# Kernel optimization log

Measured on AMD Instinct MI355X. Metric: run time of the kernel, lower is better.

## Reference

```python
import jax, jax.numpy as jnp
import numpy as np
from jax import lax

B, C, H, W = 4, 256, 64, 64
C8 = C // 8  # 32


def setup_inputs() -> dict:
    key = jax.random.key(0)
    ks = jax.random.split(key, 8)
    x = jax.random.normal(ks[0], (B, C, H, W), jnp.float32)
    # 1x1 conv weights stored as [out_ch, in_ch]
    wb = jax.random.normal(ks[1], (C8, 2 * C), jnp.float32) * 0.02
    bb = jax.random.normal(ks[2], (C8,), jnp.float32) * 0.02
    wc = jax.random.normal(ks[3], (C8, 2 * C), jnp.float32) * 0.02
    bc = jax.random.normal(ks[4], (C8,), jnp.float32) * 0.02
    wd = jax.random.normal(ks[5], (C, 2 * C), jnp.float32) * 0.02
    bd = jax.random.normal(ks[6], (C,), jnp.float32) * 0.02
    alpha = jnp.float32(0.5)  # nn.Parameter(zeros(1)) at init; nonzero for a meaningful test
    return {"x": x, "wb": wb, "bb": bb, "wc": wc, "bc": bc, "wd": wd, "bd": bd, "alpha": alpha}


def reference(x, wb, bb, wc, bc, wd, bd, alpha):
    b, c, h, w = x.shape
    n = h * w
    pad = [(0, 0), (0, 0), (1, 1), (1, 1)]
    # F.avg_pool2d(k=3, s=1, p=1) with count_include_pad=True -> window-sum / 9
    x_avg = lax.reduce_window(x, 0.0, lax.add, (1, 1, 3, 3), (1, 1, 1, 1), pad) / 9.0
    x_max = lax.reduce_window(x, -jnp.inf, lax.max, (1, 1, 3, 3), (1, 1, 1, 1), pad)
    cat = jnp.concatenate([x_avg, x_max], axis=1)  # [B, 2C, H, W]
    catf = cat.reshape(b, 2 * c, n)                # [B, 2C, N]
    # 1x1 convs == per-pixel linear projections
    feat_b = jnp.einsum('oc,bcn->bon', wb, catf) + bb[None, :, None]  # [B, C8, N]
    feat_c = jnp.einsum('oc,bcn->bon', wc, catf) + bc[None, :, None]  # [B, C8, N]
    feat_d = jnp.einsum('oc,bcn->bon', wd, catf) + bd[None, :, None]  # [B, C,  N]
    # attention_s = softmax(feat_b^T @ feat_c) over last dim -> [B, N, N]
    attn = jax.nn.softmax(jnp.einsum('bon,bom->bnm', feat_b, feat_c), axis=-1)
    # feat_e = feat_d @ attn^T -> [B, C, N]
    feat_e = jnp.einsum('bcn,bmn->bcm', feat_d, attn).reshape(b, c, h, w)
    return alpha * feat_e + (1.0 - alpha) * x
```

## Files before the change

kernel.cpp:

```cpp
#include <hip/hip_runtime.h>
#include <hip/hip_bf16.h>

typedef __hip_bfloat16 bf16;
typedef __attribute__((ext_vector_type(8))) short s8v;
typedef __attribute__((ext_vector_type(4))) float f4v;

__device__ __forceinline__ ushort f2u(float f) {
    bf16 h = __float2bfloat16(f);
    return *(ushort*)&h;
}


__global__ __launch_bounds__(256) void pool_kernel(const float* __restrict__ x,
                                                   ushort* __restrict__ cat) {
    __shared__ float Xs[3][64][66];
    int tid = threadIdx.x;
    int bid = blockIdx.x;
    int b = bid >> 8, h = (bid >> 2) & 63, cg = bid & 3;
    bool hasU = (h > 0), hasD = (h < 63);
    #pragma unroll
    for (int pp = 0; pp < 12; ++pp) {
        int linear = pp * 256 + tid;
        int w4 = linear & 15;
        int cs = (linear >> 4) & 63;
        int dh = linear >> 10;
        int hh = h + dh - 1;
        float4 f = {0.f, 0.f, 0.f, 0.f};
        if ((unsigned)hh < 64u)
            f = *(const float4*)(x + ((size_t)(b * 256 + cg * 64 + cs)) * 4096
                                 + hh * 64 + w4 * 4);
        Xs[dh][w4 * 4 + 0][cs] = f.x;
        Xs[dh][w4 * 4 + 1][cs] = f.y;
        Xs[dh][w4 * 4 + 2][cs] = f.z;
        Xs[dh][w4 * 4 + 3][cs] = f.w;
    }
    __syncthreads();
    int cs = tid & 63, ws = tid >> 6;
    float vs[18], vm[18];
    #pragma unroll
    for (int j = 0; j < 18; ++j) {
        int w = ws * 16 - 1 + j;
        if ((unsigned)w < 64u) {
            float u = Xs[0][w][cs], m = Xs[1][w][cs], d = Xs[2][w][cs];
            vs[j] = u + m + d;
            float mx = m;
            if (hasU) mx = fmaxf(mx, u);
            if (hasD) mx = fmaxf(mx, d);
            vm[j] = mx;
        } else { vs[j] = 0.f; vm[j] = -3.4e38f; }
    }
    size_t nb = ((size_t)b * 4096 + h * 64 + ws * 16) * 512 + cg * 64 + cs;
    #pragma unroll
    for (int i = 0; i < 16; ++i) {
        float sum = vs[i] + vs[i + 1] + vs[i + 2];
        float mx  = fmaxf(fmaxf(vm[i], vm[i + 1]), vm[i + 2]);
        cat[nb + (size_t)i * 512]       = f2u(sum * (1.f / 9.f));
        cat[nb + (size_t)i * 512 + 256] = f2u(mx);
    }
}

__global__ __launch_bounds__(256) void proj_kernel(
    const ushort* __restrict__ cat,
    const float* __restrict__ wb, const float* __restrict__ bb,
    const float* __restrict__ wc, const float* __restrict__ bc,
    const float* __restrict__ wd, const float* __restrict__ bd,
    ushort* __restrict__ Qb, ushort* __restrict__ Kb, ushort* __restrict__ Vf) {
    __shared__ __align__(16) ushort As[128][72];
    __shared__ __align__(16) ushort Wsm[64][72];
    __shared__ __align__(16) ushort Vls[64][136];
    int tid = threadIdx.x;
    int l = tid & 63, w = tid >> 6;
    int lm = l & 15, q = l >> 4;
    int wn = w & 1, wo = w >> 1;
    int row0 = blockIdx.x * 128;
    int col0 = blockIdx.y * 64;
    f4v acc[4][2];
    #pragma unroll
    for (int mt = 0; mt < 4; ++mt)
        #pragma unroll
        for (int ot = 0; ot < 2; ++ot)
            #pragma unroll
            for (int i = 0; i < 4; ++i) acc[mt][ot][i] = 0.f;

    int wrow_o = col0 + (tid >> 2);
    const float* wr = (wrow_o < 32) ? wb + (size_t)wrow_o * 512
                    : (wrow_o < 64) ? wc + (size_t)(wrow_o - 32) * 512
                                    : wd + (size_t)(wrow_o - 64) * 512;
    const ushort* arow = cat + (size_t)(row0 + (tid >> 1)) * 512 + (tid & 1) * 32;

    for (int kc = 0; kc < 8; ++kc) {
        {
            int r = tid >> 1, ko = (tid & 1) * 32;
            const ushort* src = arow + kc * 64;
            #pragma unroll
            for (int u = 0; u < 4; ++u)
                *(uint4*)&As[r][ko + u * 8] = *(const uint4*)(src + u * 8);
        }
        {
            int r = tid >> 2, ko = (tid & 3) * 16;
            const float* s = wr + kc * 64 + ko;
            ushort tmp[16];
            #pragma unroll
            for (int u = 0; u < 16; ++u) tmp[u] = f2u(s[u]);
            *(uint4*)&Wsm[r][ko]     = *(uint4*)&tmp[0];
            *(uint4*)&Wsm[r][ko + 8] = *(uint4*)&tmp[8];
        }
        __syncthreads();
        #pragma unroll
        for (int ks = 0; ks < 2; ++ks) {
            int kk = ks * 32;
            s8v a[4], bfr[2];
            #pragma unroll
            for (int mt = 0; mt < 4; ++mt)
                a[mt] = *(const s8v*)&As[wn * 64 + mt * 16 + lm][kk + q * 8];
            #pragma unroll
            for (int ot = 0; ot < 2; ++ot)
                bfr[ot] = *(const s8v*)&Wsm[wo * 32 + ot * 16 + lm][kk + q * 8];
            #pragma unroll
            for (int mt = 0; mt < 4; ++mt)
                #pragma unroll
                for (int ot = 0; ot < 2; ++ot)
                    acc[mt][ot] = __builtin_amdgcn_mfma_f32_16x16x32_bf16(
                        a[mt], bfr[ot], acc[mt][ot], 0, 0, 0);
        }
        __syncthreads();
    }
    if (col0 == 0) {
        #pragma unroll
        for (int ot = 0; ot < 2; ++ot) {
            int o = wo * 32 + ot * 16 + lm;
            float bias = (o < 32) ? bb[o] : bc[o - 32];
            #pragma unroll
            for (int mt = 0; mt < 4; ++mt) {
                int n = row0 + wn * 64 + mt * 16 + q * 4;
                if (o < 32) {
                    #pragma unroll
                    for (int r = 0; r < 4; ++r)
                        Qb[(size_t)(n + r) * 32 + o] = f2u(acc[mt][ot][r] + bias);
                } else {
                    #pragma unroll
                    for (int r = 0; r < 4; ++r)
                        Kb[(size_t)(n + r) * 32 + (o - 32)] = f2u(acc[mt][ot][r] + bias);
                }
            }
        }
    } else {
        #pragma unroll
        for (int ot = 0; ot < 2; ++ot) {
            int ol = wo * 32 + ot * 16 + lm;
            float bias = bd[col0 - 64 + ol];
            #pragma unroll
            for (int mt = 0; mt < 4; ++mt) {
                int nl = wn * 64 + mt * 16 + q * 4;
                #pragma unroll
                for (int r = 0; r < 4; ++r)
                    Vls[ol][nl + r] = f2u(acc[mt][ot][r] + bias);
            }
        }
        __syncthreads();
        int ol = tid >> 2;
        int nch = (tid & 3) * 32;
        int c = col0 - 64 + ol;
        int lmv = c & 15, cb = c >> 4;
        int bidx = row0 >> 12;
        int nglob = (row0 & 4095) + nch;
        size_t fbase = ((size_t)bidx << 20) + (size_t)(nglob >> 5) * 8192
                       + (size_t)cb * 512;
        #pragma unroll
        for (int qv = 0; qv < 4; ++qv)
            *(uint4*)(Vf + fbase + (qv * 16 + lmv) * 8)
                = *(const uint4*)&Vls[ol][nch + qv * 8];
    }
}

__global__ __launch_bounds__(256, 2) void attn_kernel(
    const ushort* __restrict__ Qb, const ushort* __restrict__ Kb,
    const ushort* __restrict__ Vf, const float* __restrict__ x,
    const float* __restrict__ alphap, float* __restrict__ out) {
    __shared__ __align__(16) ushort Ps[2][32][72];
    __shared__ float Lpart[4][32];
    __shared__ float Lrow[32];
    int tid = threadIdx.x;
    int l = tid & 63, w = tid >> 6;
    int lm = l & 15, q = l >> 4;
    int bid = blockIdx.x;
    int xcd = bid & 7;
    int b = xcd & 3;
    int mblk = (bid >> 3) + ((xcd >> 2) << 6);
    int m0 = mblk << 5;
    size_t bN = (size_t)b << 12;

    const ushort* kb  = Kb + (bN + w * 16 + lm) * 32 + q * 8;
    const ushort* vfb = Vf + ((size_t)b << 20) + (size_t)(w * 4) * 512
                        + (size_t)l * 8;

    s8v Qf[2];
    const ushort* qb = Qb + (bN + m0) * 32;
    #pragma unroll
    for (int mt = 0; mt < 2; ++mt)
        Qf[mt] = *(const s8v*)(qb + (size_t)(mt * 16 + lm) * 32 + q * 8);

    f4v acc0[4], acc1[4];
    #pragma unroll
    for (int ct = 0; ct < 4; ++ct)
        #pragma unroll
        for (int i = 0; i < 4; ++i) { acc0[ct][i] = 0.f; acc1[ct][i] = 0.f; }
    float Lacc0[4] = {0.f, 0.f, 0.f, 0.f};
    float Lacc1[4] = {0.f, 0.f, 0.f, 0.f};

    s8v kfA, kfB, vfA[8], vfB[8];
    kfA = *(const s8v*)kb;
    #pragma unroll
    for (int ct = 0; ct < 4; ++ct) {
        vfA[ct * 2 + 0] = *(const s8v*)(vfb + ct * 512);
        vfA[ct * 2 + 1] = *(const s8v*)(vfb + 8192 + ct * 512);
    }

#define TILE_BODY(TT, KF, VF, KFN, VFN, DOPF)                                     \
    {                                                                             \
        int p = (TT) & 1;                                                         \
        f4v S0 = {0.f, 0.f, 0.f, 0.f}, S1 = {0.f, 0.f, 0.f, 0.f};                 \
        S0 = __builtin_amdgcn_mfma_f32_16x16x32_bf16(Qf[0], KF, S0, 0, 0, 0);     \
        S1 = __builtin_amdgcn_mfma_f32_16x16x32_bf16(Qf[1], KF, S1, 0, 0, 0);     \
        _Pragma("unroll")                                                         \
        for (int r = 0; r < 4; ++r) {                                             \
            float e0 = __expf(fminf(S0[r], 60.f));                                \
            float e1 = __expf(fminf(S1[r], 60.f));                                \
            Lacc0[r] += e0; Lacc1[r] += e1;                                       \
            Ps[p][q * 4 + r][w * 16 + lm]      = f2u(e0);                         \
            Ps[p][16 + q * 4 + r][w * 16 + lm] = f2u(e1);                         \
        }                                                                         \
        __syncthreads();                                                          \
        if (DOPF) {                                                               \
            const ushort* vsrc = vfb + (size_t)((TT) + 1) * 16384;                \
            KFN = *(const s8v*)(kb + (size_t)((TT) + 1) * 2048);                  \
            _Pragma("unroll")                                                     \
            for (int ct = 0; ct < 4; ++ct) {                                      \
                VFN[ct * 2 + 0] = *(const s8v*)(vsrc + ct * 512);                 \
                VFN[ct * 2 + 1] = *(const s8v*)(vsrc + 8192 + ct * 512);          \
            }                                                                     \
        }                                                                         \
        s8v Af00 = *(const s8v*)&Ps[p][lm][q * 8];                                \
        s8v Af01 = *(const s8v*)&Ps[p][lm][32 + q * 8];                           \
        s8v Af10 = *(const s8v*)&Ps[p][16 + lm][q * 8];                           \
        s8v Af11 = *(const s8v*)&Ps[p][16 + lm][32 + q * 8];                      \
        _Pragma("unroll")                                                         \
        for (int ct = 0; ct < 4; ++ct) {                                          \
            acc0[ct] = __builtin_amdgcn_mfma_f32_16x16x32_bf16(Af00, VF[ct * 2 + 0], acc0[ct], 0, 0, 0); \
            acc1[ct] = __builtin_amdgcn_mfma_f32_16x16x32_bf16(Af10, VF[ct * 2 + 0], acc1[ct], 0, 0, 0); \
        }                                                                         \
        _Pragma("unroll")                                                         \
        for (int ct = 0; ct < 4; ++ct) {                                          \
            acc0[ct] = __builtin_amdgcn_mfma_f32_16x16x32_bf16(Af01, VF[ct * 2 + 1], acc0[ct], 0, 0, 0); \
            acc1[ct] = __builtin_amdgcn_mfma_f32_16x16x32_bf16(Af11, VF[ct * 2 + 1], acc1[ct], 0, 0, 0); \
        }                                                                         \
    }

    for (int t = 0; t < 64; t += 2) {
        TILE_BODY(t,     kfA, vfA, kfB, vfB, true);
        TILE_BODY(t + 1, kfB, vfB, kfA, vfA, (t + 2) < 64);
    }
#undef TILE_BODY

    #pragma unroll
    for (int r = 0; r < 4; ++r) {
        float v0 = Lacc0[r], v1 = Lacc1[r];
        #pragma unroll
        for (int off = 1; off < 16; off <<= 1) {
            v0 += __shfl_xor(v0, off, 64);
            v1 += __shfl_xor(v1, off, 64);
        }
        Lacc0[r] = v0; Lacc1[r] = v1;
    }
    if (lm == 0) {
        #pragma unroll
        for (int r = 0; r < 4; ++r) {
            Lpart[w][q * 4 + r]      = Lacc0[r];
            Lpart[w][16 + q * 4 + r] = Lacc1[r];
        }
    }
    __syncthreads();
    if (tid < 32)
        Lrow[tid] = Lpart[0][tid] + Lpart[1][tid] + Lpart[2][tid] + Lpart[3][tid];
    __syncthreads();
    float alpha = alphap[0];
    float ra = 1.f - alpha;
    #pragma unroll
    for (int mt = 0; mt < 2; ++mt) {
        float L0 = Lrow[mt * 16 + q * 4 + 0];
        float L1 = Lrow[mt * 16 + q * 4 + 1];
        float L2 = Lrow[mt * 16 + q * 4 + 2];
        float L3 = Lrow[mt * 16 + q * 4 + 3];
        #pragma unroll
        for (int ct = 0; ct < 4; ++ct) {
            f4v a = mt ? acc1[ct] : acc0[ct];
            int cc = w * 64 + ct * 16 + lm;
            size_t base = ((size_t)(b * 256 + cc)) * 4096 + m0 + mt * 16 + q * 4;
            float4 xv = *(const float4*)(x + base);
            float4 ov;
            ov.x = alpha * (a[0] / L0) + ra * xv.x;
            ov.y = alpha * (a[1] / L1) + ra * xv.y;
            ov.z = alpha * (a[2] / L2) + ra * xv.z;
            ov.w = alpha * (a[3] / L3) + ra * xv.w;
            *(float4*)(out + base) = ov;
        }
    }
}

extern "C" void kernel_launch(void* const* d_in, const int* in_sizes, int n_in,
                              void* d_out, int out_size, void* d_ws, size_t ws_size,
                              hipStream_t stream) {
    const float* x  = (const float*)d_in[0];
    const float* wb = (const float*)d_in[1];
    const float* bb = (const float*)d_in[2];
    const float* wc = (const float*)d_in[3];
    const float* bc = (const float*)d_in[4];
    const float* wd = (const float*)d_in[5];
    const float* bd = (const float*)d_in[6];
    const float* al = (const float*)d_in[7];
    float* out = (float*)d_out;

    char* ws = (char*)d_ws;
    ushort* cat = (ushort*)ws;
    ushort* Qb  = (ushort*)(ws + 16777216);
    ushort* Kb  = (ushort*)(ws + 17825792);
    ushort* Vf  = (ushort*)(ws + 18874368);

    pool_kernel<<<dim3(1024), dim3(256), 0, stream>>>(x, cat);
    proj_kernel<<<dim3(128, 5), dim3(256), 0, stream>>>(cat, wb, bb, wc, bc, wd, bd,
                                                        Qb, Kb, Vf);
    attn_kernel<<<dim3(512), dim3(256), 0, stream>>>(Qb, Kb, Vf, x, al, out);
}
```

Before: 169.1 us.

## Pre-convert weights, restructure projection tiling, and split attention K across wave halves

Adds a small kernel that converts the projection weights to bf16 once, in MFMA fragment order, so the projection kernel no longer converts fp32 weights per tile. The projection kernel now computes all 320 output channels for a 32-row block in a single pass instead of five column blocks that each re-read cat. The attention kernel moves to 512 threads with 64 query rows per block, splitting each key tile's reduction across two wave groups and combining their partial accumulators through shared memory. The aim is to raise MFMA reuse per loaded K/V fragment and cut redundant weight conversion, at the cost of extra LDS reductions, barriers and register pressure.

```diff
diff --git a/kernel.cpp b/kernel.cpp
--- a/kernel.cpp
+++ b/kernel.cpp
@@ -10,6 +10,24 @@
     return *(ushort*)&h;
 }
 
+
+__global__ __launch_bounds__(64) void wcvt_kernel(
+    const float* __restrict__ wb, const float* __restrict__ wc,
+    const float* __restrict__ wd, ushort* __restrict__ Wf) {
+    int ot = blockIdx.x;
+    int kc = blockIdx.y;
+    int l = threadIdx.x;
+    int o = ot * 16 + (l & 15);
+    int k0 = kc * 32 + (l >> 4) * 8;
+    const float* wr = (o < 32) ? wb + (size_t)o * 512
+                    : (o < 64) ? wc + (size_t)(o - 32) * 512
+                               : wd + (size_t)(o - 64) * 512;
+    float4 f0 = *(const float4*)(wr + k0);
+    float4 f1 = *(const float4*)(wr + k0 + 4);
+    ushort tmp[8] = {f2u(f0.x), f2u(f0.y), f2u(f0.z), f2u(f0.w),
+                     f2u(f1.x), f2u(f1.y), f2u(f1.z), f2u(f1.w)};
+    *(uint4*)(Wf + kc * 10240 + ot * 512 + l * 8) = *(uint4*)tmp;
+}
 
 __global__ __launch_bounds__(256) void pool_kernel(const float* __restrict__ x,
                                                    ushort* __restrict__ cat) {
@@ -59,200 +77,168 @@
     }
 }
 
-__global__ __launch_bounds__(256) void proj_kernel(
-    const ushort* __restrict__ cat,
-    const float* __restrict__ wb, const float* __restrict__ bb,
-    const float* __restrict__ wc, const float* __restrict__ bc,
-    const float* __restrict__ wd, const float* __restrict__ bd,
+__global__ __launch_bounds__(256, 2) void proj_kernel(
+    const ushort* __restrict__ cat, const ushort* __restrict__ Wf,
+    const float* __restrict__ bb, const float* __restrict__ bc,
+    const float* __restrict__ bd,
     ushort* __restrict__ Qb, ushort* __restrict__ Kb, ushort* __restrict__ Vf) {
-    __shared__ __align__(16) ushort As[128][72];
-    __shared__ __align__(16) ushort Wsm[64][72];
-    __shared__ __align__(16) ushort Vls[64][136];
+    __shared__ __align__(16) ushort As[32][72];
+    __shared__ __align__(16) ushort Vls[256][40];
     int tid = threadIdx.x;
     int l = tid & 63, w = tid >> 6;
     int lm = l & 15, q = l >> 4;
-    int wn = w & 1, wo = w >> 1;
-    int row0 = blockIdx.x * 128;
-    int col0 = blockIdx.y * 64;
-    f4v acc[4][2];
-    #pragma unroll
-    for (int mt = 0; mt < 4; ++mt)
-        #pragma unroll
-        for (int ot = 0; ot < 2; ++ot)
+    int n0 = blockIdx.x * 32;
+    f4v acc[2][5];
+    #pragma unroll
+    for (int mt = 0; mt < 2; ++mt)
+        #pragma unroll
+        for (int ot = 0; ot < 5; ++ot)
             #pragma unroll
             for (int i = 0; i < 4; ++i) acc[mt][ot][i] = 0.f;
 
-    int wrow_o = col0 + (tid >> 2);
-    const float* wr = (wrow_o < 32) ? wb + (size_t)wrow_o * 512
-                    : (wrow_o < 64) ? wc + (size_t)(wrow_o - 32) * 512
-                                    : wd + (size_t)(wrow_o - 64) * 512;
-    const ushort* arow = cat + (size_t)(row0 + (tid >> 1)) * 512 + (tid & 1) * 32;
+    const ushort* wfb = Wf + (w * 5) * 512 + l * 8;
+    int sr = tid >> 3, sko = (tid & 7) * 8;
+    const ushort* srow = cat + (size_t)(n0 + sr) * 512 + sko;
 
     for (int kc = 0; kc < 8; ++kc) {
-        {
-            int r = tid >> 1, ko = (tid & 1) * 32;
-            const ushort* src = arow + kc * 64;
-            #pragma unroll
-            for (int u = 0; u < 4; ++u)
-                *(uint4*)&As[r][ko + u * 8] = *(const uint4*)(src + u * 8);
-        }
-        {
-            int r = tid >> 2, ko = (tid & 3) * 16;
-            const float* s = wr + kc * 64 + ko;
-            ushort tmp[16];
-            #pragma unroll
-            for (int u = 0; u < 16; ++u) tmp[u] = f2u(s[u]);
-            *(uint4*)&Wsm[r][ko]     = *(uint4*)&tmp[0];
-            *(uint4*)&Wsm[r][ko + 8] = *(uint4*)&tmp[8];
-        }
+        *(uint4*)&As[sr][sko] = *(const uint4*)(srow + kc * 64);
         __syncthreads();
         #pragma unroll
         for (int ks = 0; ks < 2; ++ks) {
-            int kk = ks * 32;
-            s8v a[4], bfr[2];
-            #pragma unroll
-            for (int mt = 0; mt < 4; ++mt)
-                a[mt] = *(const s8v*)&As[wn * 64 + mt * 16 + lm][kk + q * 8];
-            #pragma unroll
-            for (int ot = 0; ot < 2; ++ot)
-                bfr[ot] = *(const s8v*)&Wsm[wo * 32 + ot * 16 + lm][kk + q * 8];
-            #pragma unroll
-            for (int mt = 0; mt < 4; ++mt)
-                #pragma unroll
-                for (int ot = 0; ot < 2; ++ot)
-                    acc[mt][ot] = __builtin_amdgcn_mfma_f32_16x16x32_bf16(
-                        a[mt], bfr[ot], acc[mt][ot], 0, 0, 0);
+            int kci = kc * 2 + ks;
+            s8v bf[5];
+            #pragma unroll
+            for (int ot = 0; ot < 5; ++ot)
+                bf[ot] = *(const s8v*)(wfb + kci * 10240 + ot * 512);
+            s8v a0 = *(const s8v*)&As[lm][ks * 32 + q * 8];
+            s8v a1 = *(const s8v*)&As[16 + lm][ks * 32 + q * 8];
+            #pragma unroll
+            for (int ot = 0; ot < 5; ++ot) {
+                acc[0][ot] = __builtin_amdgcn_mfma_f32_16x16x32_bf16(a0, bf[ot], acc[0][ot], 0, 0, 0);
+                acc[1][ot] = __builtin_amdgcn_mfma_f32_16x16x32_bf16(a1, bf[ot], acc[1][ot], 0, 0, 0);
+            }
         }
         __syncthreads();
     }
-    if (col0 == 0) {
-        #pragma unroll
-        for (int ot = 0; ot < 2; ++ot) {
-            int o = wo * 32 + ot * 16 + lm;
-            float bias = (o < 32) ? bb[o] : bc[o - 32];
-            #pragma unroll
-            for (int mt = 0; mt < 4; ++mt) {
-                int n = row0 + wn * 64 + mt * 16 + q * 4;
-                if (o < 32) {
-                    #pragma unroll
-                    for (int r = 0; r < 4; ++r)
-                        Qb[(size_t)(n + r) * 32 + o] = f2u(acc[mt][ot][r] + bias);
-                } else {
-                    #pragma unroll
-                    for (int r = 0; r < 4; ++r)
-                        Kb[(size_t)(n + r) * 32 + (o - 32)] = f2u(acc[mt][ot][r] + bias);
-                }
+    #pragma unroll
+    for (int ot = 0; ot < 5; ++ot) {
+        int o = w * 80 + ot * 16 + lm;
+        if (o < 32) {
+            float bias = bb[o];
+            #pragma unroll
+            for (int mt = 0; mt < 2; ++mt)
+                #pragma unroll
+                for (int r = 0; r < 4; ++r)
+                    Qb[(size_t)(n0 + mt * 16 + q * 4 + r) * 32 + o]
+                        = f2u(acc[mt][ot][r] + bias);
+        } else if (o < 64) {
+            float bias = bc[o - 32];
+            #pragma unroll
+            for (int mt = 0; mt < 2; ++mt)
+                #pragma unroll
+                for (int r = 0; r < 4; ++r)
+                    Kb[(size_t)(n0 + mt * 16 + q * 4 + r) * 32 + (o - 32)]
+                        = f2u(acc[mt][ot][r] + bias);
+        } else {
+            int c = o - 64;
+            float bias = bd[c];
+            #pragma unroll
+            for (int mt = 0; mt < 2; ++mt) {
+                ushort tmp[4];
+                #pragma unroll
+                for (int r = 0; r < 4; ++r) tmp[r] = f2u(acc[mt][ot][r] + bias);
+                *(uint2*)&Vls[c][mt * 16 + q * 4] = *(uint2*)tmp;
             }
         }
-    } else {
-        #pragma unroll
-        for (int ot = 0; ot < 2; ++ot) {
-            int ol = wo * 32 + ot * 16 + lm;
-            float bias = bd[col0 - 64 + ol];
-            #pragma unroll
-            for (int mt = 0; mt < 4; ++mt) {
-                int nl = wn * 64 + mt * 16 + q * 4;
-                #pragma unroll
-                for (int r = 0; r < 4; ++r)
-                    Vls[ol][nl + r] = f2u(acc[mt][ot][r] + bias);
-            }
-        }
-        __syncthreads();
-        int ol = tid >> 2;
-        int nch = (tid & 3) * 32;
-        int c = col0 - 64 + ol;
-        int lmv = c & 15, cb = c >> 4;
-        int bidx = row0 >> 12;
-        int nglob = (row0 & 4095) + nch;
-        size_t fbase = ((size_t)bidx << 20) + (size_t)(nglob >> 5) * 8192
-                       + (size_t)cb * 512;
-        #pragma unroll
-        for (int qv = 0; qv < 4; ++qv)
-            *(uint4*)(Vf + fbase + (qv * 16 + lmv) * 8)
-                = *(const uint4*)&Vls[ol][nch + qv * 8];
-    }
-}
-
-__global__ __launch_bounds__(256, 2) void attn_kernel(
+    }
+    __syncthreads();
+    {
+        int bidx = n0 >> 12;
+        size_t fb = ((size_t)bidx << 20) + (size_t)((n0 & 4095) >> 5) * 8192 + l * 8;
+        #pragma unroll
+        for (int i = 0; i < 4; ++i) {
+            int cb = w * 4 + i;
+            *(uint4*)(Vf + fb + cb * 512) = *(const uint4*)&Vls[cb * 16 + lm][q * 8];
+        }
+    }
+}
+
+__global__ __launch_bounds__(512, 2) void attn_kernel(
     const ushort* __restrict__ Qb, const ushort* __restrict__ Kb,
     const ushort* __restrict__ Vf, const float* __restrict__ x,
     const float* __restrict__ alphap, float* __restrict__ out) {
-    __shared__ __align__(16) ushort Ps[2][32][72];
-    __shared__ float Lpart[4][32];
-    __shared__ float Lrow[32];
+    __shared__ __align__(16) ushort Ps[2][64][72];
+    __shared__ float Obuf[4][64][17];
+    __shared__ float Lpart[4][64];
+    __shared__ float Lrow[64];
     int tid = threadIdx.x;
     int l = tid & 63, w = tid >> 6;
     int lm = l & 15, q = l >> 4;
+    int nsw = w & 3, kh = w >> 2;
     int bid = blockIdx.x;
     int xcd = bid & 7;
     int b = xcd & 3;
-    int mblk = (bid >> 3) + ((xcd >> 2) << 6);
-    int m0 = mblk << 5;
+    int midx = (bid >> 3) + ((xcd >> 2) << 5);
+    int m0 = midx << 6;
     size_t bN = (size_t)b << 12;
 
-    const ushort* kb  = Kb + (bN + w * 16 + lm) * 32 + q * 8;
-    const ushort* vfb = Vf + ((size_t)b << 20) + (size_t)(w * 4) * 512
-                        + (size_t)l * 8;
-
     s8v Qf[2];
-    const ushort* qb = Qb + (bN + m0) * 32;
-    #pragma unroll
-    for (int mt = 0; mt < 2; ++mt)
-        Qf[mt] = *(const s8v*)(qb + (size_t)(mt * 16 + lm) * 32 + q * 8);
-
-    f4v acc0[4], acc1[4];
-    #pragma unroll
-    for (int ct = 0; ct < 4; ++ct)
-        #pragma unroll
-        for (int i = 0; i < 4; ++i) { acc0[ct][i] = 0.f; acc1[ct][i] = 0.f; }
-    float Lacc0[4] = {0.f, 0.f, 0.f, 0.f};
-    float Lacc1[4] = {0.f, 0.f, 0.f, 0.f};
-
-    s8v kfA, kfB, vfA[8], vfB[8];
-    kfA = *(const s8v*)kb;
-    #pragma unroll
-    for (int ct = 0; ct < 4; ++ct) {
-        vfA[ct * 2 + 0] = *(const s8v*)(vfb + ct * 512);
-        vfA[ct * 2 + 1] = *(const s8v*)(vfb + 8192 + ct * 512);
-    }
+    {
+        const ushort* qb = Qb + (bN + m0 + kh * 32) * 32;
+        Qf[0] = *(const s8v*)(qb + (size_t)(lm) * 32 + q * 8);
+        Qf[1] = *(const s8v*)(qb + (size_t)(16 + lm) * 32 + q * 8);
+    }
+    const ushort* kbp = Kb + (bN + nsw * 16 + lm) * 32 + q * 8;
+    const ushort* vfp = Vf + ((size_t)b << 20) + kh * 8192 + (nsw * 4) * 512 + l * 8;
+
+    f4v acc[4][4];
+    #pragma unroll
+    for (int mt = 0; mt < 4; ++mt)
+        #pragma unroll
+        for (int ct = 0; ct < 4; ++ct)
+            #pragma unroll
+            for (int i = 0; i < 4; ++i) acc[mt][ct][i] = 0.f;
+    float La0 = 0.f, La1 = 0.f;
+
+    s8v kfA, kfB, vfA[4], vfB[4];
+    kfA = *(const s8v*)kbp;
+    #pragma unroll
+    for (int ct = 0; ct < 4; ++ct) vfA[ct] = *(const s8v*)(vfp + ct * 512);
 
 #define TILE_BODY(TT, KF, VF, KFN, VFN, DOPF)                                     \
     {                                                                             \
         int p = (TT) & 1;                                                         \
         f4v S0 = {0.f, 0.f, 0.f, 0.f}, S1 = {0.f, 0.f, 0.f, 0.f};                 \
-        S0 = __builtin_amdgcn_mfma_f32_16x16x32_bf16(Qf[0], KF, S0, 0, 0, 0);     \
-        S1 = __builtin_amdgcn_mfma_f32_16x16x32_bf16(Qf[1], KF, S1, 0, 0, 0);     \
+        S0 = __builtin_amdgcn_mfma_f32_16x16x32_bf16(KF, Qf[0], S0, 0, 0, 0);     \
+        S1 = __builtin_amdgcn_mfma_f32_16x16x32_bf16(KF, Qf[1], S1, 0, 0, 0);     \
+        ushort e0[4], e1[4];                                                      \
         _Pragma("unroll")                                                         \
         for (int r = 0; r < 4; ++r) {                                             \
-            float e0 = __expf(fminf(S0[r], 60.f));                                \
-            float e1 = __expf(fminf(S1[r], 60.f));                                \
-            Lacc0[r] += e0; Lacc1[r] += e1;                                       \
-            Ps[p][q * 4 + r][w * 16 + lm]      = f2u(e0);                         \
-            Ps[p][16 + q * 4 + r][w * 16 + lm] = f2u(e1);                         \
+            float f0 = __expf(fminf(S0[r], 60.f));                                \
+            float f1 = __expf(fminf(S1[r], 60.f));                                \
+            La0 += f0; La1 += f1;                                                 \
+            e0[r] = f2u(f0); e1[r] = f2u(f1);                                     \
         }                                                                         \
+        *(uint2*)&Ps[p][kh * 32 + lm][nsw * 16 + q * 4]      = *(uint2*)e0;       \
+        *(uint2*)&Ps[p][kh * 32 + 16 + lm][nsw * 16 + q * 4] = *(uint2*)e1;       \
         __syncthreads();                                                          \
         if (DOPF) {                                                               \
-            const ushort* vsrc = vfb + (size_t)((TT) + 1) * 16384;                \
-            KFN = *(const s8v*)(kb + (size_t)((TT) + 1) * 2048);                  \
+            KFN = *(const s8v*)(kbp + (size_t)((TT) + 1) * 2048);                 \
+            const ushort* vn = vfp + (size_t)((TT) + 1) * 16384;                  \
             _Pragma("unroll")                                                     \
-            for (int ct = 0; ct < 4; ++ct) {                                      \
-                VFN[ct * 2 + 0] = *(const s8v*)(vsrc + ct * 512);                 \
-                VFN[ct * 2 + 1] = *(const s8v*)(vsrc + 8192 + ct * 512);          \
-            }                                                                     \
+            for (int ct = 0; ct < 4; ++ct)                                        \
+                VFN[ct] = *(const s8v*)(vn + ct * 512);                           \
         }                                                                         \
-        s8v Af00 = *(const s8v*)&Ps[p][lm][q * 8];                                \
-        s8v Af01 = *(const s8v*)&Ps[p][lm][32 + q * 8];                           \
-        s8v Af10 = *(const s8v*)&Ps[p][16 + lm][q * 8];                           \
-        s8v Af11 = *(const s8v*)&Ps[p][16 + lm][32 + q * 8];                      \
+        s8v Af0 = *(const s8v*)&Ps[p][lm][kh * 32 + q * 8];                       \
+        s8v Af1 = *(const s8v*)&Ps[p][16 + lm][kh * 32 + q * 8];                  \
+        s8v Af2 = *(const s8v*)&Ps[p][32 + lm][kh * 32 + q * 8];                  \
+        s8v Af3 = *(const s8v*)&Ps[p][48 + lm][kh * 32 + q * 8];                  \
         _Pragma("unroll")                                                         \
         for (int ct = 0; ct < 4; ++ct) {                                          \
-            acc0[ct] = __builtin_amdgcn_mfma_f32_16x16x32_bf16(Af00, VF[ct * 2 + 0], acc0[ct], 0, 0, 0); \
-            acc1[ct] = __builtin_amdgcn_mfma_f32_16x16x32_bf16(Af10, VF[ct * 2 + 0], acc1[ct], 0, 0, 0); \
-        }                                                                         \
-        _Pragma("unroll")                                                         \
-        for (int ct = 0; ct < 4; ++ct) {                                          \
-            acc0[ct] = __builtin_amdgcn_mfma_f32_16x16x32_bf16(Af01, VF[ct * 2 + 1], acc0[ct], 0, 0, 0); \
-            acc1[ct] = __builtin_amdgcn_mfma_f32_16x16x32_bf16(Af11, VF[ct * 2 + 1], acc1[ct], 0, 0, 0); \
+            acc[0][ct] = __builtin_amdgcn_mfma_f32_16x16x32_bf16(Af0, VF[ct], acc[0][ct], 0, 0, 0); \
+            acc[1][ct] = __builtin_amdgcn_mfma_f32_16x16x32_bf16(Af1, VF[ct], acc[1][ct], 0, 0, 0); \
+            acc[2][ct] = __builtin_amdgcn_mfma_f32_16x16x32_bf16(Af2, VF[ct], acc[2][ct], 0, 0, 0); \
+            acc[3][ct] = __builtin_amdgcn_mfma_f32_16x16x32_bf16(Af3, VF[ct], acc[3][ct], 0, 0, 0); \
         }                                                                         \
     }
 
@@ -262,47 +248,56 @@
     }
 #undef TILE_BODY
 
-    #pragma unroll
-    for (int r = 0; r < 4; ++r) {
-        float v0 = Lacc0[r], v1 = Lacc1[r];
-        #pragma unroll
-        for (int off = 1; off < 16; off <<= 1) {
-            v0 += __shfl_xor(v0, off, 64);
-            v1 += __shfl_xor(v1, off, 64);
-        }
-        Lacc0[r] = v0; Lacc1[r] = v1;
-    }
-    if (lm == 0) {
-        #pragma unroll
-        for (int r = 0; r < 4; ++r) {
-            Lpart[w][q * 4 + r]      = Lacc0[r];
-            Lpart[w][16 + q * 4 + r] = Lacc1[r];
-        }
+    La0 += __shfl_xor(La0, 16, 64); La0 += __shfl_xor(La0, 32, 64);
+    La1 += __shfl_xor(La1, 16, 64); La1 += __shfl_xor(La1, 32, 64);
+    if (q == 0) {
+        Lpart[nsw][kh * 32 + lm]      = La0;
+        Lpart[nsw][kh * 32 + 16 + lm] = La1;
     }
     __syncthreads();
-    if (tid < 32)
+    if (tid < 64)
         Lrow[tid] = Lpart[0][tid] + Lpart[1][tid] + Lpart[2][tid] + Lpart[3][tid];
     __syncthreads();
-    float alpha = alphap[0];
-    float ra = 1.f - alpha;
-    #pragma unroll
-    for (int mt = 0; mt < 2; ++mt) {
-        float L0 = Lrow[mt * 16 + q * 4 + 0];
-        float L1 = Lrow[mt * 16 + q * 4 + 1];
-        float L2 = Lrow[mt * 16 + q * 4 + 2];
-        float L3 = Lrow[mt * 16 + q * 4 + 3];
-        #pragma unroll
-        for (int ct = 0; ct < 4; ++ct) {
-            f4v a = mt ? acc1[ct] : acc0[ct];
-            int cc = w * 64 + ct * 16 + lm;
-            size_t base = ((size_t)(b * 256 + cc)) * 4096 + m0 + mt * 16 + q * 4;
-            float4 xv = *(const float4*)(x + base);
-            float4 ov;
-            ov.x = alpha * (a[0] / L0) + ra * xv.x;
-            ov.y = alpha * (a[1] / L1) + ra * xv.y;
-            ov.z = alpha * (a[2] / L2) + ra * xv.z;
-            ov.w = alpha * (a[3] / L3) + ra * xv.w;
-            *(float4*)(out + base) = ov;
+    #pragma unroll
+    for (int ct = 0; ct < 4; ++ct) {
+        if (kh == 1) {
+            #pragma unroll
+            for (int mt = 0; mt < 4; ++mt)
+                #pragma unroll
+                for (int r = 0; r < 4; ++r)
+                    Obuf[nsw][mt * 16 + q * 4 + r][lm] = acc[mt][ct][r];
+        }
+        __syncthreads();
+        if (kh == 0) {
+            #pragma unroll
+            for (int mt = 0; mt < 4; ++mt)
+                #pragma unroll
+                for (int r = 0; r < 4; ++r)
+                    acc[mt][ct][r] += Obuf[nsw][mt * 16 + q * 4 + r][lm];
+        }
+        __syncthreads();
+    }
+    if (kh == 0) {
+        float alpha = alphap[0];
+        float ra = 1.f - alpha;
+        #pragma unroll
+        for (int mt = 0; mt < 4; ++mt) {
+            float L0 = Lrow[mt * 16 + q * 4 + 0];
+            float L1 = Lrow[mt * 16 + q * 4 + 1];
+            float L2 = Lrow[mt * 16 + q * 4 + 2];
+            float L3 = Lrow[mt * 16 + q * 4 + 3];
+            #pragma unroll
+            for (int ct = 0; ct < 4; ++ct) {
+                int cc = nsw * 64 + ct * 16 + lm;
+                size_t base = ((size_t)(b * 256 + cc)) * 4096 + m0 + mt * 16 + q * 4;
+                float4 xv = *(const float4*)(x + base);
+                float4 ov;
+                ov.x = alpha * (acc[mt][ct][0] / L0) + ra * xv.x;
+                ov.y = alpha * (acc[mt][ct][1] / L1) + ra * xv.y;
+                ov.z = alpha * (acc[mt][ct][2] / L2) + ra * xv.z;
+                ov.w = alpha * (acc[mt][ct][3] / L3) + ra * xv.w;
+                *(float4*)(out + base) = ov;
+            }
         }
     }
 }
@@ -325,9 +320,11 @@
     ushort* Qb  = (ushort*)(ws + 16777216);
     ushort* Kb  = (ushort*)(ws + 17825792);
     ushort* Vf  = (ushort*)(ws + 18874368);
-
+    ushort* Wf  = (ushort*)(ws + 27262976);
+
+    wcvt_kernel<<<dim3(20, 16), dim3(64), 0, stream>>>(wb, wc, wd, Wf);
     pool_kernel<<<dim3(1024), dim3(256), 0, stream>>>(x, cat);
-    proj_kernel<<<dim3(128, 5), dim3(256), 0, stream>>>(cat, wb, bb, wc, bc, wd, bd,
-                                                        Qb, Kb, Vf);
-    attn_kernel<<<dim3(512), dim3(256), 0, stream>>>(Qb, Kb, Vf, x, al, out);
-}
+    proj_kernel<<<dim3(512), dim3(256), 0, stream>>>(cat, Wf, bb, bc, bd,
+                                                     Qb, Kb, Vf);
+    attn_kernel<<<dim3(256), dim3(512), 0, stream>>>(Qb, Kb, Vf, x, al, out);
+}
```

Result: no change. 171.8 us (+1.6%).
